# Performance work log

Measured on AMD Instinct MI355X. Metric: run time of the kernel, lower is better.

The kernel has to match this reference:

```python
import jax, jax.numpy as jnp
import numpy as np

N = 27            # hardcoded node count in the module
D = 1024          # state_dim
E = D * 5         # MHA embed dim = 5120
H = 4             # n_heads


def setup_inputs() -> dict:
    key = jax.random.key(0)
    ks = jax.random.split(key, 6)
    s = 0.02
    return {
        "node_states": jax.random.normal(ks[0], (N, D, 5), jnp.float32),
        "hist_prev": jax.random.normal(ks[1], (N, D, 5), jnp.float32),
        "granger_w": jax.random.normal(ks[2], (1, 2 * E), jnp.float32) * s,
        "granger_b": jnp.zeros((1,), jnp.float32),
        "in_proj_w": jax.random.normal(ks[3], (3 * E, E), jnp.float32) * s,
        "in_proj_b": jnp.zeros((3 * E,), jnp.float32),
        "out_proj_w": jax.random.normal(ks[4], (E, E), jnp.float32) * s,
        "out_proj_b": jnp.zeros((E,), jnp.float32),
        "light_hertz": 500,
    }


def _mha(x, in_w, in_b, out_w, out_b):
    # x: [N, E]; torch MultiheadAttention with q=k=v=x, batch of 1
    qkv = x @ in_w.T + in_b                       # [N, 3E]
    q, k, v = jnp.split(qkv, 3, axis=-1)          # each [N, E]
    hd = E // H
    q = q.reshape(N, H, hd).transpose(1, 0, 2)    # [H, N, hd]
    k = k.reshape(N, H, hd).transpose(1, 0, 2)
    v = v.reshape(N, H, hd).transpose(1, 0, 2)
    scores = jnp.einsum('hqd,hkd->hqk', q, k) / jnp.sqrt(jnp.float32(hd))
    attn = jax.nn.softmax(scores, axis=-1)        # [H, N, N]
    o = jnp.einsum('hqk,hkd->hqd', attn, v)       # [H, N, hd]
    o = o.transpose(1, 0, 2).reshape(N, E)
    return o @ out_w.T + out_b                    # [N, E]


def reference(node_states, hist_prev, granger_w, granger_b,
              in_proj_w, in_proj_b, out_proj_w, out_proj_b, light_hertz):
    node_flat = node_states.reshape(N, E)         # [N, E]
    hist_flat = hist_prev.reshape(N, E)           # [N, E]

    # Granger pairwise test, vectorized: pred_input = [hist[j], node[i]]
    # score[i, j] = sigmoid(hist[j] . w_h + node[i] . w_n + b)
    w_h = granger_w[0, :E]
    w_n = granger_w[0, E:]
    col = node_flat @ w_n                          # [N] -> varies with i
    row = hist_flat @ w_h                          # [N] -> varies with j
    adj = jax.nn.sigmoid(col[:, None] + row[None, :] + granger_b[0])  # [N, N]
    causal_adj = adj * (1.0 - jnp.eye(N, dtype=adj.dtype))            # zero diagonal

    hertz_weight = jnp.clip(jnp.float32(light_hertz) / 1000.0, 0.1, 1.0)
    attended = _mha(node_flat, in_proj_w, in_proj_b, out_proj_w, out_proj_b)
    out = (attended * hertz_weight).reshape(N, D, 5)
    return out, causal_adj
```

## Files before the change

### kernel.cpp

```cpp
#include <hip/hip_runtime.h>

#define NROW 27
#define EDIM 5120
#define QKVDIM 15360
#define HD 1280

#define BN 256
#define BM 32
#define KC 32

__global__ __launch_bounds__(256)
void gemm_tall(const float* __restrict__ X, const float* __restrict__ W,
               float* __restrict__ C, const float* __restrict__ bias,
               const int* __restrict__ hz, int K, int Ntot, int Kc)
{
    __shared__ float Ws[KC][BN];
    __shared__ float Xs[KC][BM];

    const int tid = threadIdx.x;
    const int n0  = blockIdx.x * BN;
    const int k0  = blockIdx.y * Kc;

    const int tn = tid & 63;
    const int tm = tid >> 6;

    float acc[8][4];
    #pragma unroll
    for (int mi = 0; mi < 8; ++mi)
        #pragma unroll
        for (int ni = 0; ni < 4; ++ni) acc[mi][ni] = 0.f;

    const float* wrow = W + (size_t)(n0 + tid) * K + k0;
    const int  mx  = tid & 31;
    const int  k4x = tid >> 5;
    const bool xok = (mx < NROW);
    const float* xrow = X + (size_t)(xok ? mx : 0) * K + k0 + 4 * k4x;

    for (int kb = 0; kb < Kc; kb += KC) {
        #pragma unroll
        for (int it = 0; it < 8; ++it) {
            float4 w4 = *(const float4*)(wrow + 4 * it);
            Ws[4*it+0][tid] = w4.x;
            Ws[4*it+1][tid] = w4.y;
            Ws[4*it+2][tid] = w4.z;
            Ws[4*it+3][tid] = w4.w;
        }
        float4 x4 = xok ? *(const float4*)xrow : make_float4(0.f, 0.f, 0.f, 0.f);
        Xs[4*k4x+0][mx] = x4.x;
        Xs[4*k4x+1][mx] = x4.y;
        Xs[4*k4x+2][mx] = x4.z;
        Xs[4*k4x+3][mx] = x4.w;
        __syncthreads();

        #pragma unroll 8
        for (int kc = 0; kc < KC; ++kc) {
            float4 wv = *(const float4*)&Ws[kc][4 * tn];
            float4 xa = *(const float4*)&Xs[kc][8 * tm];
            float4 xb = *(const float4*)&Xs[kc][8 * tm + 4];
            float xv[8] = {xa.x, xa.y, xa.z, xa.w, xb.x, xb.y, xb.z, xb.w};
            float wvv[4] = {wv.x, wv.y, wv.z, wv.w};
            #pragma unroll
            for (int mi = 0; mi < 8; ++mi)
                #pragma unroll
                for (int ni = 0; ni < 4; ++ni)
                    acc[mi][ni] = fmaf(xv[mi], wvv[ni], acc[mi][ni]);
        }
        __syncthreads();
        wrow += KC;
        xrow += KC;
    }

    float scale = 1.0f;
    if (hz) {
        float h = (float)hz[0] * 0.001f;
        scale = fminf(fmaxf(h, 0.1f), 1.0f);
    }
    const bool addb = (bias != nullptr) && (blockIdx.y == 0);
    #pragma unroll
    for (int mi = 0; mi < 8; ++mi) {
        int m = 8 * tm + mi;
        if (m < NROW) {
            #pragma unroll
            for (int ni = 0; ni < 4; ++ni) {
                int n = n0 + 4 * tn + ni;
                float v = acc[mi][ni];
                if (addb) v += bias[n];
                atomicAdd(&C[(size_t)m * Ntot + n], v * scale);
            }
        }
    }
}

__global__ __launch_bounds__(256)
void colrow_kernel(const float* __restrict__ node, const float* __restrict__ hist,
                   const float* __restrict__ gw, float* __restrict__ cr)
{
    const int b = blockIdx.x;
    const float* x = (b < NROW) ? node + (size_t)b * EDIM : hist + (size_t)(b - NROW) * EDIM;
    const float* w = (b < NROW) ? gw + EDIM : gw;
    const int tid = threadIdx.x;
    float a = 0.f;
    for (int f = tid; f < EDIM / 4; f += 256) {
        float4 xv = ((const float4*)x)[f];
        float4 wv = ((const float4*)w)[f];
        a += xv.x * wv.x + xv.y * wv.y + xv.z * wv.z + xv.w * wv.w;
    }
    #pragma unroll
    for (int off = 32; off; off >>= 1) a += __shfl_down(a, off);
    __shared__ float red[4];
    if ((tid & 63) == 0) red[tid >> 6] = a;
    __syncthreads();
    if (tid == 0) cr[b] = red[0] + red[1] + red[2] + red[3];
}

__global__ void adj_kernel(const float* __restrict__ cr, const float* __restrict__ gb,
                           float* __restrict__ adj)
{
    const int t = threadIdx.x;
    if (t < NROW * NROW) {
        const int i = t / NROW, j = t % NROW;
        float v = 0.f;
        if (i != j) {
            float z = cr[i] + cr[NROW + j] + gb[0];
            v = 1.0f / (1.0f + expf(-z));
        }
        adj[t] = v;
    }
}

__global__ __launch_bounds__(256)
void attn_kernel(const float* __restrict__ qkv, float* __restrict__ O)
{
    __shared__ float qs[HD];
    __shared__ float sc[NROW];
    __shared__ float pr[NROW];
    const int bx = blockIdx.x;
    const int h = bx & 3;
    const int i = bx >> 2;
    const int tid = threadIdx.x;

    const size_t qoff = (size_t)i * QKVDIM + (size_t)h * HD;
    for (int d = tid; d < HD; d += 256) qs[d] = qkv[qoff + d];
    __syncthreads();

    const int wid = tid >> 6, lane = tid & 63;
    for (int j = wid; j < NROW; j += 4) {
        const float* kr = qkv + (size_t)j * QKVDIM + EDIM + (size_t)h * HD;
        float a = 0.f;
        #pragma unroll
        for (int it = 0; it < 5; ++it) {
            int d4 = lane + 64 * it;
            float4 k4 = *(const float4*)(kr + 4 * d4);
            float4 q4 = *(const float4*)(qs + 4 * d4);
            a += q4.x * k4.x + q4.y * k4.y + q4.z * k4.z + q4.w * k4.w;
        }
        #pragma unroll
        for (int off = 32; off; off >>= 1) a += __shfl_down(a, off);
        if (lane == 0) sc[j] = a * 0.02795084971874737f;
    }
    __syncthreads();

    float mxv = -1e30f;
    for (int j = 0; j < NROW; ++j) mxv = fmaxf(mxv, sc[j]);
    float s = 0.f;
    for (int j = 0; j < NROW; ++j) s += expf(sc[j] - mxv);
    if (tid < NROW) pr[tid] = expf(sc[tid] - mxv) / s;
    __syncthreads();

    for (int d4 = tid; d4 < HD / 4; d4 += 256) {
        float4 o = make_float4(0.f, 0.f, 0.f, 0.f);
        for (int j = 0; j < NROW; ++j) {
            const float4 v4 = *(const float4*)(qkv + (size_t)j * QKVDIM + 2 * EDIM + (size_t)h * HD + 4 * d4);
            const float p = pr[j];
            o.x = fmaf(p, v4.x, o.x);
            o.y = fmaf(p, v4.y, o.y);
            o.z = fmaf(p, v4.z, o.z);
            o.w = fmaf(p, v4.w, o.w);
        }
        *(float4*)(O + (size_t)i * EDIM + (size_t)h * HD + 4 * d4) = o;
    }
}

extern "C" void kernel_launch(void* const* d_in, const int* in_sizes, int n_in,
                              void* d_out, int out_size, void* d_ws, size_t ws_size,
                              hipStream_t stream)
{
    const float* node = (const float*)d_in[0];
    const float* hist = (const float*)d_in[1];
    const float* gw   = (const float*)d_in[2];
    const float* gb   = (const float*)d_in[3];
    const float* inw  = (const float*)d_in[4];
    const float* inb  = (const float*)d_in[5];
    const float* outw = (const float*)d_in[6];
    const float* outb = (const float*)d_in[7];
    const int*   hz   = (const int*)d_in[8];

    float* out  = (float*)d_out;
    float* qkvf = (float*)d_ws;
    float* Obuf = qkvf + (size_t)NROW * QKVDIM;
    float* cr   = Obuf + (size_t)NROW * EDIM;

    hipMemsetAsync(qkvf, 0, sizeof(float) * NROW * QKVDIM, stream);
    hipMemsetAsync(out, 0, sizeof(float) * NROW * EDIM, stream);

    colrow_kernel<<<54, 256, 0, stream>>>(node, hist, gw, cr);
    adj_kernel<<<1, 768, 0, stream>>>(cr, gb, out + (size_t)NROW * EDIM);

    gemm_tall<<<dim3(60, 8), 256, 0, stream>>>(node, inw, qkvf, inb, nullptr,
                                               EDIM, QKVDIM, EDIM / 8);
    attn_kernel<<<108, 256, 0, stream>>>(qkvf, Obuf);
    gemm_tall<<<dim3(20, 16), 256, 0, stream>>>(Obuf, outw, out, outb, hz,
                                                EDIM, EDIM, EDIM / 16);
}
```

Measured before the change: 641.4 us.

## Use split-bf16 MFMA GEMMs with partial buffers and a reduce pass

Both projection GEMMs are replaced with a kernel that splits each fp32 value into high and low bf16 parts and runs three MFMA 16x16x32 products per tile (hi*hi, hi*lo, lo*hi) to keep close to fp32 accuracy. The atomic-add split-K epilogue and the memsets are replaced by per-split partial buffers written to workspace, followed by a separate reduce kernel that adds the bias and hertz scale. This targets the scalar-FMA compute and atomic traffic. In exchange it adds conversion work, extra workspace traffic for the partials, two more launches, and a small precision loss from the dropped lo*lo term.

```diff
diff --git a/kernel.cpp b/kernel.cpp
--- a/kernel.cpp
+++ b/kernel.cpp
@@ -5,90 +5,161 @@
 #define QKVDIM 15360
 #define HD 1280
 
-#define BN 256
-#define BM 32
-#define KC 32
-
-__global__ __launch_bounds__(256)
-void gemm_tall(const float* __restrict__ X, const float* __restrict__ W,
-               float* __restrict__ C, const float* __restrict__ bias,
-               const int* __restrict__ hz, int K, int Ntot, int Kc)
-{
-    __shared__ float Ws[KC][BN];
-    __shared__ float Xs[KC][BM];
+typedef __attribute__((ext_vector_type(8))) short bf16x8;
+typedef __attribute__((ext_vector_type(4))) float f32x4;
+
+__device__ inline short f2bf(float x) {
+    unsigned u = __builtin_bit_cast(unsigned, x);
+    u = (u + 0x7FFFu + ((u >> 16) & 1u)) >> 16;
+    return (short)u;
+}
+__device__ inline float bf2f(short h) {
+    unsigned u = ((unsigned)(unsigned short)h) << 16;
+    return __builtin_bit_cast(float, u);
+}
+
+#define KC 64
+#define LDK 72
+
+__global__ __launch_bounds__(256)
+void gemm_bf16x2(const float* __restrict__ X, const float* __restrict__ W,
+                 float* __restrict__ Cp, int K, int Ntot, int Kblk)
+{
+    __shared__ short Whi[128][LDK];
+    __shared__ short Wlo[128][LDK];
+    __shared__ short Xhi[32][LDK];
+    __shared__ short Xlo[32][LDK];
 
     const int tid = threadIdx.x;
-    const int n0  = blockIdx.x * BN;
-    const int k0  = blockIdx.y * Kc;
-
-    const int tn = tid & 63;
-    const int tm = tid >> 6;
-
-    float acc[8][4];
+    const int n0 = blockIdx.x * 128;
+    const int k0 = blockIdx.y * Kblk;
+
+    const int lane = tid & 63;
+    const int wv   = tid >> 6;
+    const int lm   = lane & 15;
+    const int q8   = (lane >> 4) * 8;
+
+    f32x4 acc[2][2] = {};
+
+    const int wr  = tid >> 1;
+    const int wkh = (tid & 1) * 32;
+    const float* wp = W + (size_t)(n0 + wr) * K + k0 + wkh;
+
+    const int xr = tid >> 3;
+    const int xk = (tid & 7) * 8;
+    const bool xok = (xr < NROW);
+    const float* xp = X + (size_t)(xok ? xr : 0) * K + k0 + xk;
+
+    for (int kc = 0; kc < Kblk; kc += KC) {
+        float wbuf[32];
+        #pragma unroll
+        for (int i = 0; i < 8; ++i)
+            *(float4*)&wbuf[4 * i] = ((const float4*)wp)[i];
+        #pragma unroll
+        for (int g = 0; g < 4; ++g) {
+            bf16x8 h8, l8;
+            #pragma unroll
+            for (int j = 0; j < 8; ++j) {
+                float f = wbuf[8 * g + j];
+                short h = f2bf(f);
+                h8[j] = h;
+                l8[j] = f2bf(f - bf2f(h));
+            }
+            *(bf16x8*)&Whi[wr][wkh + 8 * g] = h8;
+            *(bf16x8*)&Wlo[wr][wkh + 8 * g] = l8;
+        }
+        {
+            float xbuf[8];
+            if (xok) {
+                *(float4*)&xbuf[0] = ((const float4*)xp)[0];
+                *(float4*)&xbuf[4] = ((const float4*)xp)[1];
+            } else {
+                #pragma unroll
+                for (int j = 0; j < 8; ++j) xbuf[j] = 0.f;
+            }
+            bf16x8 h8, l8;
+            #pragma unroll
+            for (int j = 0; j < 8; ++j) {
+                short h = f2bf(xbuf[j]);
+                h8[j] = h;
+                l8[j] = f2bf(xbuf[j] - bf2f(h));
+            }
+            *(bf16x8*)&Xhi[xr][xk] = h8;
+            *(bf16x8*)&Xlo[xr][xk] = l8;
+        }
+        __syncthreads();
+
+        #pragma unroll
+        for (int s = 0; s < 2; ++s) {
+            const int ko = 32 * s + q8;
+            bf16x8 ah0 = *(const bf16x8*)&Xhi[lm][ko];
+            bf16x8 ah1 = *(const bf16x8*)&Xhi[lm + 16][ko];
+            bf16x8 al0 = *(const bf16x8*)&Xlo[lm][ko];
+            bf16x8 al1 = *(const bf16x8*)&Xlo[lm + 16][ko];
+            bf16x8 bh0 = *(const bf16x8*)&Whi[32 * wv + lm][ko];
+            bf16x8 bh1 = *(const bf16x8*)&Whi[32 * wv + 16 + lm][ko];
+            bf16x8 bl0 = *(const bf16x8*)&Wlo[32 * wv + lm][ko];
+            bf16x8 bl1 = *(const bf16x8*)&Wlo[32 * wv + 16 + lm][ko];
+
+            acc[0][0] = __builtin_amdgcn_mfma_f32_16x16x32_bf16(ah0, bh0, acc[0][0], 0, 0, 0);
+            acc[0][0] = __builtin_amdgcn_mfma_f32_16x16x32_bf16(ah0, bl0, acc[0][0], 0, 0, 0);
+            acc[0][0] = __builtin_amdgcn_mfma_f32_16x16x32_bf16(al0, bh0, acc[0][0], 0, 0, 0);
+
+            acc[0][1] = __builtin_amdgcn_mfma_f32_16x16x32_bf16(ah0, bh1, acc[0][1], 0, 0, 0);
+            acc[0][1] = __builtin_amdgcn_mfma_f32_16x16x32_bf16(ah0, bl1, acc[0][1], 0, 0, 0);
+            acc[0][1] = __builtin_amdgcn_mfma_f32_16x16x32_bf16(al0, bh1, acc[0][1], 0, 0, 0);
+
+            acc[1][0] = __builtin_amdgcn_mfma_f32_16x16x32_bf16(ah1, bh0, acc[1][0], 0, 0, 0);
+            acc[1][0] = __builtin_amdgcn_mfma_f32_16x16x32_bf16(ah1, bl0, acc[1][0], 0, 0, 0);
+            acc[1][0] = __builtin_amdgcn_mfma_f32_16x16x32_bf16(al1, bh0, acc[1][0], 0, 0, 0);
+
+            acc[1][1] = __builtin_amdgcn_mfma_f32_16x16x32_bf16(ah1, bh1, acc[1][1], 0, 0, 0);
+            acc[1][1] = __builtin_amdgcn_mfma_f32_16x16x32_bf16(ah1, bl1, acc[1][1], 0, 0, 0);
+            acc[1][1] = __builtin_amdgcn_mfma_f32_16x16x32_bf16(al1, bh1, acc[1][1], 0, 0, 0);
+        }
+        __syncthreads();
+        wp += KC;
+        xp += KC;
+    }
+
+    const size_t base = (size_t)blockIdx.y * NROW * Ntot;
     #pragma unroll
-    for (int mi = 0; mi < 8; ++mi)
-        #pragma unroll
-        for (int ni = 0; ni < 4; ++ni) acc[mi][ni] = 0.f;
-
-    const float* wrow = W + (size_t)(n0 + tid) * K + k0;
-    const int  mx  = tid & 31;
-    const int  k4x = tid >> 5;
-    const bool xok = (mx < NROW);
-    const float* xrow = X + (size_t)(xok ? mx : 0) * K + k0 + 4 * k4x;
-
-    for (int kb = 0; kb < Kc; kb += KC) {
-        #pragma unroll
-        for (int it = 0; it < 8; ++it) {
-            float4 w4 = *(const float4*)(wrow + 4 * it);
-            Ws[4*it+0][tid] = w4.x;
-            Ws[4*it+1][tid] = w4.y;
-            Ws[4*it+2][tid] = w4.z;
-            Ws[4*it+3][tid] = w4.w;
-        }
-        float4 x4 = xok ? *(const float4*)xrow : make_float4(0.f, 0.f, 0.f, 0.f);
-        Xs[4*k4x+0][mx] = x4.x;
-        Xs[4*k4x+1][mx] = x4.y;
-        Xs[4*k4x+2][mx] = x4.z;
-        Xs[4*k4x+3][mx] = x4.w;
-        __syncthreads();
-
-        #pragma unroll 8
-        for (int kc = 0; kc < KC; ++kc) {
-            float4 wv = *(const float4*)&Ws[kc][4 * tn];
-            float4 xa = *(const float4*)&Xs[kc][8 * tm];
-            float4 xb = *(const float4*)&Xs[kc][8 * tm + 4];
-            float xv[8] = {xa.x, xa.y, xa.z, xa.w, xb.x, xb.y, xb.z, xb.w};
-            float wvv[4] = {wv.x, wv.y, wv.z, wv.w};
-            #pragma unroll
-            for (int mi = 0; mi < 8; ++mi)
+    for (int mi = 0; mi < 2; ++mi) {
+        #pragma unroll
+        for (int r = 0; r < 4; ++r) {
+            const int m = mi * 16 + (lane >> 4) * 4 + r;
+            if (m < NROW) {
                 #pragma unroll
-                for (int ni = 0; ni < 4; ++ni)
-                    acc[mi][ni] = fmaf(xv[mi], wvv[ni], acc[mi][ni]);
-        }
-        __syncthreads();
-        wrow += KC;
-        xrow += KC;
-    }
-
-    float scale = 1.0f;
+                for (int ni = 0; ni < 2; ++ni) {
+                    const int n = n0 + 32 * wv + ni * 16 + lm;
+                    Cp[base + (size_t)m * Ntot + n] = acc[mi][ni][r];
+                }
+            }
+        }
+    }
+}
+
+__global__ __launch_bounds__(256)
+void reduce_kernel(const float* __restrict__ Cp, const float* __restrict__ bias,
+                   float* __restrict__ out, int Ntot, int nky, const int* __restrict__ hz)
+{
+    const int idx = blockIdx.x * 256 + threadIdx.x;
+    const int total4 = NROW * Ntot / 4;
+    if (idx >= total4) return;
+    float4 s = ((const float4*)Cp)[idx];
+    for (int k = 1; k < nky; ++k) {
+        float4 p = ((const float4*)(Cp + (size_t)k * NROW * Ntot))[idx];
+        s.x += p.x; s.y += p.y; s.z += p.z; s.w += p.w;
+    }
+    const int n = (idx * 4) % Ntot;
+    float4 b = *(const float4*)(bias + n);
+    s.x += b.x; s.y += b.y; s.z += b.z; s.w += b.w;
     if (hz) {
         float h = (float)hz[0] * 0.001f;
-        scale = fminf(fmaxf(h, 0.1f), 1.0f);
-    }
-    const bool addb = (bias != nullptr) && (blockIdx.y == 0);
-    #pragma unroll
-    for (int mi = 0; mi < 8; ++mi) {
-        int m = 8 * tm + mi;
-        if (m < NROW) {
-            #pragma unroll
-            for (int ni = 0; ni < 4; ++ni) {
-                int n = n0 + 4 * tn + ni;
-                float v = acc[mi][ni];
-                if (addb) v += bias[n];
-                atomicAdd(&C[(size_t)m * Ntot + n], v * scale);
-            }
-        }
-    }
+        float sc = fminf(fmaxf(h, 0.1f), 1.0f);
+        s.x *= sc; s.y *= sc; s.z *= sc; s.w *= sc;
+    }
+    ((float4*)out)[idx] = s;
 }
 
 __global__ __launch_bounds__(256)
@@ -195,20 +266,22 @@
     const float* outb = (const float*)d_in[7];
     const int*   hz   = (const int*)d_in[8];
 
-    float* out  = (float*)d_out;
-    float* qkvf = (float*)d_ws;
+    float* out = (float*)d_out;
+
+    float* Cp1  = (float*)d_ws;
+    float* qkvf = Cp1 + (size_t)4 * NROW * QKVDIM;
     float* Obuf = qkvf + (size_t)NROW * QKVDIM;
-    float* cr   = Obuf + (size_t)NROW * EDIM;
-
-    hipMemsetAsync(qkvf, 0, sizeof(float) * NROW * QKVDIM, stream);
-    hipMemsetAsync(out, 0, sizeof(float) * NROW * EDIM, stream);
+    float* Cp2  = Obuf + (size_t)NROW * EDIM;
+    float* cr   = Cp2 + (size_t)8 * NROW * EDIM;
 
     colrow_kernel<<<54, 256, 0, stream>>>(node, hist, gw, cr);
     adj_kernel<<<1, 768, 0, stream>>>(cr, gb, out + (size_t)NROW * EDIM);
 
-    gemm_tall<<<dim3(60, 8), 256, 0, stream>>>(node, inw, qkvf, inb, nullptr,
-                                               EDIM, QKVDIM, EDIM / 8);
+    gemm_bf16x2<<<dim3(120, 4), 256, 0, stream>>>(node, inw, Cp1, EDIM, QKVDIM, EDIM / 4);
+    reduce_kernel<<<(NROW * QKVDIM / 4 + 255) / 256, 256, 0, stream>>>(Cp1, inb, qkvf, QKVDIM, 4, nullptr);
+
     attn_kernel<<<108, 256, 0, stream>>>(qkvf, Obuf);
-    gemm_tall<<<dim3(20, 16), 256, 0, stream>>>(Obuf, outw, out, outb, hz,
-                                                EDIM, EDIM, EDIM / 16);
-}
+
+    gemm_bf16x2<<<dim3(40, 8), 256, 0, stream>>>(Obuf, outw, Cp2, EDIM, EDIM, EDIM / 8);
+    reduce_kernel<<<(NROW * EDIM / 4 + 255) / 256, 256, 0, stream>>>(Cp2, outb, out, EDIM, 8, hz);
+}
```

Result: faster. 550.2 us (-14.2%).
